# Kernel optimization log

Hardware: AMD Instinct MI355X
Metric: run time of the kernel (lower is better)

Reference implementation:

```python
import jax, jax.numpy as jnp
import numpy as np

N_HEAD = 8
LN_EPS = 1e-5


def _ln(z, g, b):
    m = jnp.mean(z, axis=-1, keepdims=True)
    v = jnp.var(z, axis=-1, keepdims=True)
    return (z - m) / jnp.sqrt(v + LN_EPS) * g + b


def setup_inputs() -> dict:
    key = jax.random.key(0)
    ks = jax.random.split(key, 20)
    B, N, H, F = 4, 256, 128, 512
    p = {}
    p["x"] = jax.random.normal(ks[0], (B, N, H), dtype=jnp.float32)
    p["e"] = jax.random.normal(ks[1], (B, N, N, H), dtype=jnp.float32)
    p["attention_mask"] = jnp.zeros((B, N_HEAD, N, N), dtype=jnp.float32)
    s = 0.02
    p["Wq"] = jax.random.normal(ks[2], (H, H)) * s; p["bq"] = jnp.zeros((H,))
    p["Wk"] = jax.random.normal(ks[3], (H, H)) * s; p["bk"] = jnp.zeros((H,))
    p["Wv"] = jax.random.normal(ks[4], (H, H)) * s; p["bv"] = jnp.zeros((H,))
    p["We"] = jax.random.normal(ks[5], (H, H)) * s; p["be"] = jnp.zeros((H,))
    p["Woh"] = jax.random.normal(ks[6], (H, H)) * s; p["boh"] = jnp.zeros((H,))
    p["Woe"] = jax.random.normal(ks[7], (H, H)) * s; p["boe"] = jnp.zeros((H,))
    p["Wf1x"] = jax.random.normal(ks[8], (H, F)) * s; p["bf1x"] = jnp.zeros((F,))
    p["Wf2x"] = jax.random.normal(ks[9], (F, H)) * s; p["bf2x"] = jnp.zeros((H,))
    p["Wf1e"] = jax.random.normal(ks[10], (H, F)) * s; p["bf1e"] = jnp.zeros((F,))
    p["Wf2e"] = jax.random.normal(ks[11], (F, H)) * s; p["bf2e"] = jnp.zeros((H,))
    p["g1x"] = jnp.ones((H,)); p["b1x"] = jnp.zeros((H,))
    p["g1e"] = jnp.ones((H,)); p["b1e"] = jnp.zeros((H,))
    return p


def reference(x, e, attention_mask, Wq, bq, Wk, bk, Wv, bv, We, be,
              Woh, boh, Woe, boe, Wf1x, bf1x, Wf2x, bf2x,
              Wf1e, bf1e, Wf2e, bf2e, g1x, b1x, g1e, b1e):
    B, N, H = x.shape
    h = N_HEAD
    d = H // h
    # projections; NOTE: V uses the K projection (faithful to original bug)
    Qx = (x @ Wq + bq).reshape(B, N, h, d).transpose(0, 2, 1, 3)   # (B,h,N,d)
    Kx = (x @ Wk + bk).reshape(B, N, h, d).transpose(0, 2, 1, 3)
    Vx = (x @ Wk + bk).reshape(B, N, h, d).transpose(0, 2, 1, 3)
    Ee = (e @ We + be).reshape(B, N, N, h, d).transpose(0, 3, 1, 2, 4)  # (B,h,N,N,d)
    scale = 1.0 / np.sqrt(d).astype(np.float32)
    inter = Qx[:, :, :, None, :] * Kx[:, :, None, :, :] * Ee * scale   # (B,h,N,N,d)
    scores = jax.nn.softmax(attention_mask + inter.sum(-1), axis=-1)   # (B,h,N,N)
    e_attn = inter.transpose(0, 2, 3, 1, 4).reshape(B, N, N, H) @ Woe + boe
    att = jnp.einsum('bhij,bhjd->bhid', scores, Vx)
    x_attn = att.transpose(0, 2, 1, 3).reshape(B, N, H) @ Woh + boh
    # residual + layernorm (original 'layer' path reuses normalization1_* twice)
    x1 = _ln(x_attn + x, g1x, b1x)
    e1 = _ln(e_attn + e, g1e, b1e)
    x_ff = jax.nn.relu(x1 @ Wf1x + bf1x) @ Wf2x + bf2x
    e_ff = jax.nn.relu(e1 @ Wf1e + bf1e) @ Wf2e + bf2e
    x2 = _ln(x_ff + x1, g1x, b1x)
    e2 = _ln(e_ff + e1, g1e, b1e)
    return x2, e2
```

## Files before the change

### kernel.cpp

```cpp
#include <hip/hip_runtime.h>
#include <math.h>

#define NSEQ 256
#define HD 128
#define FD 512
#define NHD 8
#define LNEPS 1e-5f

typedef __attribute__((ext_vector_type(8))) short bf16x8;
typedef __attribute__((ext_vector_type(4))) float f32x4;

__device__ __forceinline__ unsigned short f2bf(float x) {
  union { float f; unsigned int u; } v; v.f = x;
  unsigned int r = v.u + 0x7fffu + ((v.u >> 16) & 1u);
  return (unsigned short)(r >> 16);
}

__device__ __forceinline__ float bf2f(unsigned short u) {
  union { float f; unsigned int v; } cv; cv.v = ((unsigned int)u) << 16;
  return cv.f;
}

__global__ void prep_weights(const float* __restrict__ W1f, const float* __restrict__ W2f,
                             unsigned short* __restrict__ W1T, unsigned short* __restrict__ W2T) {
  int t = blockIdx.x * 256 + threadIdx.x;
  int tot = gridDim.x * 256;
  for (int idx = t; idx < FD * HD; idx += tot) {
    int n = idx >> 7, k = idx & (HD - 1);
    W1T[idx] = f2bf(W1f[k * FD + n]);
  }
  for (int idx = t; idx < HD * FD; idx += tot) {
    int n = idx >> 9, k = idx & (FD - 1);
    W2T[idx] = f2bf(W2f[k * HD + n]);
  }
}

__global__ __launch_bounds__(128) void qk_proj(const float* __restrict__ x,
    const float* __restrict__ Wq, const float* __restrict__ bq,
    const float* __restrict__ Wk, const float* __restrict__ bk,
    float* __restrict__ Qs, float* __restrict__ Kp) {
  int row = blockIdx.x;
  int c = threadIdx.x;
  __shared__ float xl[HD];
  xl[c] = x[row * HD + c];
  __syncthreads();
  float aq = bq[c], ak = bk[c];
  #pragma unroll 8
  for (int k = 0; k < HD; ++k) {
    float xv = xl[k];
    aq = fmaf(xv, Wq[k * HD + c], aq);
    ak = fmaf(xv, Wk[k * HD + c], ak);
  }
  Qs[row * HD + c] = aq * 0.25f;
  Kp[row * HD + c] = ak;
}

__global__ __launch_bounds__(256) void edge_attn(
    const float* __restrict__ e,
    const float* __restrict__ We, const float* __restrict__ be,
    const float* __restrict__ Woe, const float* __restrict__ boe,
    const float* __restrict__ Qs, const float* __restrict__ Kp,
    const float* __restrict__ g1e, const float* __restrict__ b1e,
    float* __restrict__ Sout, float* __restrict__ e1out) {
  const int gid = blockIdx.x;
  const int jt = gid & 3, i = (gid >> 2) & (NSEQ - 1), b = gid >> 10;
  const int j0 = jt * 64;
  const int t = threadIdx.x;
  const int w = t >> 6, l = t & 63;
  const int wr = w >> 1, wc = w & 1;
  const int l15 = l & 15, lg = l >> 4;

  __shared__ unsigned short eL[64 * 128];
  __shared__ unsigned short kL[64 * 136];
  __shared__ float qL[HD], beL[HD], boeL[HD], gL[HD], bbL[HD];
  __shared__ float redS[64][2], redQ[64][2];

  if (t < HD) {
    qL[t]   = Qs[(b * NSEQ + i) * HD + t];
    beL[t]  = be[t];
    boeL[t] = boe[t];
    gL[t]   = g1e[t];
    bbL[t]  = b1e[t];
  }
  const int ebase = ((b * NSEQ + i) * NSEQ + j0) * HD;
  for (int v = t; v < 64 * 16; v += 256) {
    int r = v >> 4, c8 = (v & 15) << 3;
    const float* se = &e[ebase + r * HD + c8];
    float4 e0 = *(const float4*)se;
    float4 e1v = *(const float4*)(se + 4);
    union { bf16x8 v8; unsigned short u[8]; } pk;
    pk.u[0] = f2bf(e0.x); pk.u[1] = f2bf(e0.y); pk.u[2] = f2bf(e0.z); pk.u[3] = f2bf(e0.w);
    pk.u[4] = f2bf(e1v.x); pk.u[5] = f2bf(e1v.y); pk.u[6] = f2bf(e1v.z); pk.u[7] = f2bf(e1v.w);
    *(bf16x8*)&eL[r * HD + (c8 ^ ((r & 7) << 3))] = pk.v8;
    const float* sk = &Kp[(b * NSEQ + j0 + r) * HD + c8];
    float4 k0 = *(const float4*)sk;
    float4 k1 = *(const float4*)(sk + 4);
    pk.u[0] = f2bf(k0.x); pk.u[1] = f2bf(k0.y); pk.u[2] = f2bf(k0.z); pk.u[3] = f2bf(k0.w);
    pk.u[4] = f2bf(k1.x); pk.u[5] = f2bf(k1.y); pk.u[6] = f2bf(k1.z); pk.u[7] = f2bf(k1.w);
    *(bf16x8*)&kL[r * 136 + c8] = pk.v8;
  }
  __syncthreads();

  f32x4 acc1[2][4];
  #pragma unroll
  for (int tm = 0; tm < 2; ++tm)
    #pragma unroll
    for (int tn = 0; tn < 4; ++tn) {
      float bv = beL[wc * 64 + tn * 16 + l15];
      acc1[tm][tn] = (f32x4){bv, bv, bv, bv};
    }
  #pragma unroll
  for (int ks = 0; ks < 4; ++ks) {
    bf16x8 af[2], bfr[4];
    #pragma unroll
    for (int tm = 0; tm < 2; ++tm) {
      int mrow = wr * 32 + tm * 16 + l15;
      af[tm] = *(const bf16x8*)&eL[mrow * HD + ((ks * 32 + lg * 8) ^ ((mrow & 7) << 3))];
    }
    #pragma unroll
    for (int tn = 0; tn < 4; ++tn) {
      int n = wc * 64 + tn * 16 + l15;
      const float* wp = &We[(ks * 32 + lg * 8) * HD + n];
      union { bf16x8 v8; unsigned short u[8]; } pk;
      #pragma unroll
      for (int ii = 0; ii < 8; ++ii) pk.u[ii] = f2bf(wp[ii * HD]);
      bfr[tn] = pk.v8;
    }
    #pragma unroll
    for (int tm = 0; tm < 2; ++tm)
      #pragma unroll
      for (int tn = 0; tn < 4; ++tn)
        acc1[tm][tn] = __builtin_amdgcn_mfma_f32_16x16x32_bf16(af[tm], bfr[tn], acc1[tm][tn], 0, 0, 0);
  }

  #pragma unroll
  for (int tm = 0; tm < 2; ++tm)
    #pragma unroll
    for (int tn = 0; tn < 4; ++tn) {
      int c = wc * 64 + tn * 16 + l15;
      float qv = qL[c];
      f32x4 p;
      #pragma unroll
      for (int ii = 0; ii < 4; ++ii) {
        int r = wr * 32 + tm * 16 + lg * 4 + ii;
        p[ii] = acc1[tm][tn][ii] * qv * bf2f(kL[r * 136 + c]);
      }
      acc1[tm][tn] = p;
      float h0 = p[0], h1 = p[1], h2 = p[2], h3 = p[3];
      #pragma unroll
      for (int off = 1; off < 16; off <<= 1) {
        h0 += __shfl_xor(h0, off); h1 += __shfl_xor(h1, off);
        h2 += __shfl_xor(h2, off); h3 += __shfl_xor(h3, off);
      }
      if (l15 < 4) {
        float val = l15 == 0 ? h0 : l15 == 1 ? h1 : l15 == 2 ? h2 : h3;
        int r = wr * 32 + tm * 16 + lg * 4 + l15;
        Sout[((b * NHD + (wc * 4 + tn)) * NSEQ + i) * NSEQ + j0 + r] = val;
      }
    }
  __syncthreads();

  #pragma unroll
  for (int tm = 0; tm < 2; ++tm)
    #pragma unroll
    for (int tn = 0; tn < 4; ++tn) {
      int c = wc * 64 + tn * 16 + l15;
      #pragma unroll
      for (int ii = 0; ii < 4; ++ii) {
        int r = wr * 32 + tm * 16 + lg * 4 + ii;
        eL[r * HD + (c ^ ((r & 7) << 3))] = f2bf(acc1[tm][tn][ii]);
      }
    }
  __syncthreads();

  f32x4 acc2[2][4];
  #pragma unroll
  for (int tm = 0; tm < 2; ++tm)
    #pragma unroll
    for (int tn = 0; tn < 4; ++tn) {
      float bv = boeL[wc * 64 + tn * 16 + l15];
      acc2[tm][tn] = (f32x4){bv, bv, bv, bv};
    }
  #pragma unroll
  for (int ks = 0; ks < 4; ++ks) {
    bf16x8 af[2], bfr[4];
    #pragma unroll
    for (int tm = 0; tm < 2; ++tm) {
      int mrow = wr * 32 + tm * 16 + l15;
      af[tm] = *(const bf16x8*)&eL[mrow * HD + ((ks * 32 + lg * 8) ^ ((mrow & 7) << 3))];
    }
    #pragma unroll
    for (int tn = 0; tn < 4; ++tn) {
      int n = wc * 64 + tn * 16 + l15;
      const float* wp = &Woe[(ks * 32 + lg * 8) * HD + n];
      union { bf16x8 v8; unsigned short u[8]; } pk;
      #pragma unroll
      for (int ii = 0; ii < 8; ++ii) pk.u[ii] = f2bf(wp[ii * HD]);
      bfr[tn] = pk.v8;
    }
    #pragma unroll
    for (int tm = 0; tm < 2; ++tm)
      #pragma unroll
      for (int tn = 0; tn < 4; ++tn)
        acc2[tm][tn] = __builtin_amdgcn_mfma_f32_16x16x32_bf16(af[tm], bfr[tn], acc2[tm][tn], 0, 0, 0);
  }

  #pragma unroll
  for (int tm = 0; tm < 2; ++tm) {
    #pragma unroll
    for (int tn = 0; tn < 4; ++tn) {
      int c = wc * 64 + tn * 16 + l15;
      #pragma unroll
      for (int ii = 0; ii < 4; ++ii) {
        int r = wr * 32 + tm * 16 + lg * 4 + ii;
        acc2[tm][tn][ii] += e[ebase + r * HD + c];
      }
    }
    #pragma unroll
    for (int ii = 0; ii < 4; ++ii) {
      float s  = acc2[tm][0][ii] + acc2[tm][1][ii] + acc2[tm][2][ii] + acc2[tm][3][ii];
      float sq = acc2[tm][0][ii] * acc2[tm][0][ii] + acc2[tm][1][ii] * acc2[tm][1][ii]
               + acc2[tm][2][ii] * acc2[tm][2][ii] + acc2[tm][3][ii] * acc2[tm][3][ii];
      #pragma unroll
      for (int off = 1; off < 16; off <<= 1) {
        s += __shfl_xor(s, off); sq += __shfl_xor(sq, off);
      }
      if (l15 == 0) {
        int r = wr * 32 + tm * 16 + lg * 4 + ii;
        redS[r][wc] = s; redQ[r][wc] = sq;
      }
    }
  }
  __syncthreads();

  #pragma unroll
  for (int tm = 0; tm < 2; ++tm) {
    float mrow[4], rsrow[4];
    #pragma unroll
    for (int ii = 0; ii < 4; ++ii) {
      int r = wr * 32 + tm * 16 + lg * 4 + ii;
      float s = redS[r][0] + redS[r][1];
      float sq = redQ[r][0] + redQ[r][1];
      float m = s * (1.f / HD);
      float var = sq * (1.f / HD) - m * m;
      mrow[ii] = m; rsrow[ii] = rsqrtf(var + LNEPS);
    }
    #pragma unroll
    for (int tn = 0; tn < 4; ++tn) {
      int c = wc * 64 + tn * 16 + l15;
      float gv = gL[c], bv = bbL[c];
      #pragma unroll
      for (int ii = 0; ii < 4; ++ii) {
        int r = wr * 32 + tm * 16 + lg * 4 + ii;
        e1out[ebase + r * HD + c] = (acc2[tm][tn][ii] - mrow[ii]) * rsrow[ii] * gv + bv;
      }
    }
  }
}

__global__ __launch_bounds__(256) void softmax_k(float* __restrict__ S,
    const float* __restrict__ mask) {
  int row = blockIdx.x;
  int t = threadIdx.x;
  int idx = row * NSEQ + t;
  float v = S[idx] + mask[idx];
  float m = v;
  #pragma unroll
  for (int off = 1; off < 64; off <<= 1) m = fmaxf(m, __shfl_xor(m, off));
  __shared__ float wbuf[8];
  if ((t & 63) == 0) wbuf[t >> 6] = m;
  __syncthreads();
  m = fmaxf(fmaxf(wbuf[0], wbuf[1]), fmaxf(wbuf[2], wbuf[3]));
  float ex = __expf(v - m);
  float s = ex;
  #pragma unroll
  for (int off = 1; off < 64; off <<= 1) s += __shfl_xor(s, off);
  __syncthreads();
  if ((t & 63) == 0) wbuf[4 + (t >> 6)] = s;
  __syncthreads();
  s = wbuf[4] + wbuf[5] + wbuf[6] + wbuf[7];
  S[idx] = ex / s;
}

__global__ __launch_bounds__(128) void x_attn_ln(
    const float* __restrict__ x, const float* __restrict__ scores,
    const float* __restrict__ Kp,
    const float* __restrict__ Woh, const float* __restrict__ boh,
    const float* __restrict__ g1x, const float* __restrict__ b1x,
    float* __restrict__ x1out) {
  int bi = blockIdx.x; int b = bi >> 8; int i = bi & 255;
  int c = threadIdx.x;
  __shared__ float sL[NHD * NSEQ];
  __shared__ float attL[HD];
  __shared__ float rbuf[4];

  for (int v = c; v < NHD * NSEQ; v += 128) {
    int h = v >> 8, j = v & 255;
    sL[v] = scores[((b * NHD + h) * NSEQ + i) * NSEQ + j];
  }
  __syncthreads();
  int h = c >> 4;
  float att = 0.f;
  for (int j = 0; j < NSEQ; ++j)
    att = fmaf(sL[h * NSEQ + j], Kp[(b * NSEQ + j) * HD + c], att);
  attL[c] = att;
  __syncthreads();
  float o = boh[c];
  for (int k = 0; k < HD; ++k) o = fmaf(attL[k], Woh[k * HD + c], o);
  o += x[bi * HD + c];
  float s = o, s2 = o * o;
  #pragma unroll
  for (int off = 1; off < 64; off <<= 1) { s += __shfl_xor(s, off); s2 += __shfl_xor(s2, off); }
  if ((c & 63) == 0) { rbuf[(c >> 6) * 2] = s; rbuf[(c >> 6) * 2 + 1] = s2; }
  __syncthreads();
  s = rbuf[0] + rbuf[2]; s2 = rbuf[1] + rbuf[3];
  float m = s * (1.f / HD);
  float var = s2 * (1.f / HD) - m * m;
  x1out[bi * HD + c] = (o - m) * rsqrtf(var + LNEPS) * g1x[c] + b1x[c];
}

__global__ __launch_bounds__(256) void ffn_mfma(
    const float* in1,
    const unsigned short* __restrict__ W1T, const float* __restrict__ b1,
    const unsigned short* __restrict__ W2T, const float* __restrict__ b2,
    const float* __restrict__ g, const float* __restrict__ bb,
    float* out2) {
  const int row0 = blockIdx.x * 64;
  const int t = threadIdx.x;
  const int w = t >> 6, l = t & 63;
  const int wr = w >> 1, wc = w & 1;
  const int l15 = l & 15, lg = l >> 4;

  __shared__ __align__(16) char smem[34816];
  unsigned short* aL = (unsigned short*)smem;
  unsigned short* hL = (unsigned short*)(smem + 16384);
  float* b1L = (float*)(smem + 32768);
  float* epi = (float*)smem;

  for (int v = t; v < 64 * 16; v += 256) {
    int r = v >> 4, c8 = (v & 15) << 3;
    const float* src = &in1[(row0 + r) * HD + c8];
    float4 f0 = *(const float4*)src;
    float4 f1 = *(const float4*)(src + 4);
    union { bf16x8 v8; unsigned short u[8]; } pk;
    pk.u[0] = f2bf(f0.x); pk.u[1] = f2bf(f0.y); pk.u[2] = f2bf(f0.z); pk.u[3] = f2bf(f0.w);
    pk.u[4] = f2bf(f1.x); pk.u[5] = f2bf(f1.y); pk.u[6] = f2bf(f1.z); pk.u[7] = f2bf(f1.w);
    *(bf16x8*)&aL[r * HD + (c8 ^ ((r & 7) << 3))] = pk.v8;
  }
  for (int v = t; v < FD; v += 256) b1L[v] = b1[v];
  __syncthreads();

  f32x4 acc2[2][4];
  #pragma unroll
  for (int tm = 0; tm < 2; ++tm)
    #pragma unroll
    for (int tn = 0; tn < 4; ++tn) acc2[tm][tn] = (f32x4){0.f, 0.f, 0.f, 0.f};

  for (int fc = 0; fc < 4; ++fc) {
    f32x4 acc1[2][4];
    #pragma unroll
    for (int tm = 0; tm < 2; ++tm)
      #pragma unroll
      for (int tn = 0; tn < 4; ++tn) acc1[tm][tn] = (f32x4){0.f, 0.f, 0.f, 0.f};
    #pragma unroll
    for (int ks = 0; ks < 4; ++ks) {
      bf16x8 af[2], bfr[4];
      #pragma unroll
      for (int tm = 0; tm < 2; ++tm) {
        int mrow = wr * 32 + tm * 16 + l15;
        af[tm] = *(const bf16x8*)&aL[mrow * HD + ((ks * 32 + lg * 8) ^ ((mrow & 7) << 3))];
      }
      #pragma unroll
      for (int tn = 0; tn < 4; ++tn) {
        int n = fc * 128 + wc * 64 + tn * 16 + l15;
        bfr[tn] = *(const bf16x8*)&W1T[n * HD + ks * 32 + lg * 8];
      }
      #pragma unroll
      for (int tm = 0; tm < 2; ++tm)
        #pragma unroll
        for (int tn = 0; tn < 4; ++tn)
          acc1[tm][tn] = __builtin_amdgcn_mfma_f32_16x16x32_bf16(af[tm], bfr[tn], acc1[tm][tn], 0, 0, 0);
    }
    __syncthreads();
    #pragma unroll
    for (int tm = 0; tm < 2; ++tm)
      #pragma unroll
      for (int tn = 0; tn < 4; ++tn) {
        int col = wc * 64 + tn * 16 + l15;
        float bias = b1L[fc * 128 + col];
        #pragma unroll
        for (int ii = 0; ii < 4; ++ii) {
          int r = wr * 32 + tm * 16 + lg * 4 + ii;
          float hv = fmaxf(acc1[tm][tn][ii] + bias, 0.f);
          hL[r * HD + (col ^ ((r & 7) << 3))] = f2bf(hv);
        }
      }
    __syncthreads();
    #pragma unroll
    for (int ks = 0; ks < 4; ++ks) {
      bf16x8 af[2], bfr[4];
      #pragma unroll
      for (int tm = 0; tm < 2; ++tm) {
        int mrow = wr * 32 + tm * 16 + l15;
        af[tm] = *(const bf16x8*)&hL[mrow * HD + ((ks * 32 + lg * 8) ^ ((mrow & 7) << 3))];
      }
      #pragma unroll
      for (int tn = 0; tn < 4; ++tn) {
        int n = wc * 64 + tn * 16 + l15;
        bfr[tn] = *(const bf16x8*)&W2T[n * FD + fc * 128 + ks * 32 + lg * 8];
      }
      #pragma unroll
      for (int tm = 0; tm < 2; ++tm)
        #pragma unroll
        for (int tn = 0; tn < 4; ++tn)
          acc2[tm][tn] = __builtin_amdgcn_mfma_f32_16x16x32_bf16(af[tm], bfr[tn], acc2[tm][tn], 0, 0, 0);
    }
  }

  float res[2][4][4];
  #pragma unroll
  for (int tm = 0; tm < 2; ++tm)
    #pragma unroll
    for (int tn = 0; tn < 4; ++tn) {
      int col = wc * 64 + tn * 16 + l15;
      #pragma unroll
      for (int ii = 0; ii < 4; ++ii) {
        int r = wr * 32 + tm * 16 + lg * 4 + ii;
        res[tm][tn][ii] = bf2f(aL[r * HD + (col ^ ((r & 7) << 3))]);
      }
    }
  __syncthreads();

  #pragma unroll
  for (int tm = 0; tm < 2; ++tm)
    #pragma unroll
    for (int tn = 0; tn < 4; ++tn) {
      int col = wc * 64 + tn * 16 + l15;
      float bias = b2[col];
      #pragma unroll
      for (int ii = 0; ii < 4; ++ii) {
        int r = wr * 32 + tm * 16 + lg * 4 + ii;
        epi[r * 132 + col] = acc2[tm][tn][ii] + bias + res[tm][tn][ii];
      }
    }
  __syncthreads();
  {
    int r = t >> 2, sgi = t & 3;
    const float* rowp = &epi[r * 132 + sgi * 32];
    float sum = 0.f, sq = 0.f;
    #pragma unroll
    for (int u = 0; u < 32; u += 4) {
      float4 v4 = *(const float4*)&rowp[u];
      sum += v4.x + v4.y + v4.z + v4.w;
      sq  += v4.x * v4.x + v4.y * v4.y + v4.z * v4.z + v4.w * v4.w;
    }
    sum += __shfl_xor(sum, 1); sq += __shfl_xor(sq, 1);
    sum += __shfl_xor(sum, 2); sq += __shfl_xor(sq, 2);
    float m = sum * (1.f / HD);
    float var = sq * (1.f / HD) - m * m;
    float rs = rsqrtf(var + LNEPS);
    #pragma unroll
    for (int u = 0; u < 32; u += 4) {
      float4 v4 = *(const float4*)&rowp[u];
      int cb = sgi * 32 + u;
      float4 o;
      o.x = (v4.x - m) * rs * g[cb + 0] + bb[cb + 0];
      o.y = (v4.y - m) * rs * g[cb + 1] + bb[cb + 1];
      o.z = (v4.z - m) * rs * g[cb + 2] + bb[cb + 2];
      o.w = (v4.w - m) * rs * g[cb + 3] + bb[cb + 3];
      *(float4*)&out2[(row0 + r) * HD + cb] = o;
    }
  }
}

__global__ __launch_bounds__(256) void ffn_mfma_e(
    const float* in1,
    const float* __restrict__ W1, const float* __restrict__ b1,
    const float* __restrict__ W2, const float* __restrict__ b2,
    const float* __restrict__ g, const float* __restrict__ bb,
    float* out2) {
  const int t = threadIdx.x;
  const int w = t >> 6, l = t & 63;
  const int wr = w >> 1, wc = w & 1;
  const int l15 = l & 15, lg = l >> 4;
  const int rowbase = blockIdx.x * 512;

  __shared__ __align__(16) char smem[69632];
  unsigned short* aL = (unsigned short*)smem;
  unsigned short* hL = (unsigned short*)(smem + 16384);
  float* b1L = (float*)(smem + 32768);
  float* epi = (float*)(smem + 34816);

  for (int v = t; v < FD; v += 256) b1L[v] = b1[v];

  for (int ch = 0; ch < 8; ++ch) {
    const int row0 = rowbase + ch * 64;
    __syncthreads();

    for (int v = t; v < 64 * 16; v += 256) {
      int r = v >> 4, c8 = (v & 15) << 3;
      const float* src = &in1[(row0 + r) * HD + c8];
      float4 f0 = *(const float4*)src;
      float4 f1 = *(const float4*)(src + 4);
      union { bf16x8 v8; unsigned short u[8]; } pk;
      pk.u[0] = f2bf(f0.x); pk.u[1] = f2bf(f0.y); pk.u[2] = f2bf(f0.z); pk.u[3] = f2bf(f0.w);
      pk.u[4] = f2bf(f1.x); pk.u[5] = f2bf(f1.y); pk.u[6] = f2bf(f1.z); pk.u[7] = f2bf(f1.w);
      *(bf16x8*)&aL[r * HD + (c8 ^ ((r & 7) << 3))] = pk.v8;
    }
    __syncthreads();

    f32x4 acc2[2][4];
    #pragma unroll
    for (int tm = 0; tm < 2; ++tm)
      #pragma unroll
      for (int tn = 0; tn < 4; ++tn) acc2[tm][tn] = (f32x4){0.f, 0.f, 0.f, 0.f};

    for (int fc = 0; fc < 4; ++fc) {
      f32x4 acc1[2][4];
      #pragma unroll
      for (int tm = 0; tm < 2; ++tm)
        #pragma unroll
        for (int tn = 0; tn < 4; ++tn) acc1[tm][tn] = (f32x4){0.f, 0.f, 0.f, 0.f};
      #pragma unroll
      for (int ks = 0; ks < 4; ++ks) {
        bf16x8 af[2], bfr[4];
        #pragma unroll
        for (int tm = 0; tm < 2; ++tm) {
          int mrow = wr * 32 + tm * 16 + l15;
          af[tm] = *(const bf16x8*)&aL[mrow * HD + ((ks * 32 + lg * 8) ^ ((mrow & 7) << 3))];
        }
        #pragma unroll
        for (int tn = 0; tn < 4; ++tn) {
          int n = fc * 128 + wc * 64 + tn * 16 + l15;
          const float* wp = &W1[(ks * 32 + lg * 8) * FD + n];
          union { bf16x8 v8; unsigned short u[8]; } pk;
          #pragma unroll
          for (int i = 0; i < 8; ++i) pk.u[i] = f2bf(wp[i * FD]);
          bfr[tn] = pk.v8;
        }
        #pragma unroll
        for (int tm = 0; tm < 2; ++tm)
          #pragma unroll
          for (int tn = 0; tn < 4; ++tn)
            acc1[tm][tn] = __builtin_amdgcn_mfma_f32_16x16x32_bf16(af[tm], bfr[tn], acc1[tm][tn], 0, 0, 0);
      }
      __syncthreads();
      #pragma unroll
      for (int tm = 0; tm < 2; ++tm)
        #pragma unroll
        for (int tn = 0; tn < 4; ++tn) {
          int col = wc * 64 + tn * 16 + l15;
          float bias = b1L[fc * 128 + col];
          #pragma unroll
          for (int ii = 0; ii < 4; ++ii) {
            int r = wr * 32 + tm * 16 + lg * 4 + ii;
            float hv = fmaxf(acc1[tm][tn][ii] + bias, 0.f);
            hL[r * HD + (col ^ ((r & 7) << 3))] = f2bf(hv);
          }
        }
      __syncthreads();
      #pragma unroll
      for (int ks = 0; ks < 4; ++ks) {
        bf16x8 af[2], bfr[4];
        #pragma unroll
        for (int tm = 0; tm < 2; ++tm) {
          int mrow = wr * 32 + tm * 16 + l15;
          af[tm] = *(const bf16x8*)&hL[mrow * HD + ((ks * 32 + lg * 8) ^ ((mrow & 7) << 3))];
        }
        #pragma unroll
        for (int tn = 0; tn < 4; ++tn) {
          int n = wc * 64 + tn * 16 + l15;
          const float* wp = &W2[(fc * 128 + ks * 32 + lg * 8) * HD + n];
          union { bf16x8 v8; unsigned short u[8]; } pk;
          #pragma unroll
          for (int i = 0; i < 8; ++i) pk.u[i] = f2bf(wp[i * HD]);
          bfr[tn] = pk.v8;
        }
        #pragma unroll
        for (int tm = 0; tm < 2; ++tm)
          #pragma unroll
          for (int tn = 0; tn < 4; ++tn)
            acc2[tm][tn] = __builtin_amdgcn_mfma_f32_16x16x32_bf16(af[tm], bfr[tn], acc2[tm][tn], 0, 0, 0);
      }
    }

    #pragma unroll
    for (int tm = 0; tm < 2; ++tm)
      #pragma unroll
      for (int tn = 0; tn < 4; ++tn) {
        int col = wc * 64 + tn * 16 + l15;
        float bias = b2[col];
        #pragma unroll
        for (int ii = 0; ii < 4; ++ii) {
          int r = wr * 32 + tm * 16 + lg * 4 + ii;
          float rv = bf2f(aL[r * HD + (col ^ ((r & 7) << 3))]);
          epi[r * 132 + col] = acc2[tm][tn][ii] + bias + rv;
        }
      }
    __syncthreads();
    {
      int r = t >> 2, sgi = t & 3;
      const float* rowp = &epi[r * 132 + sgi * 32];
      float sum = 0.f, sq = 0.f;
      #pragma unroll
      for (int u = 0; u < 32; u += 4) {
        float4 v4 = *(const float4*)&rowp[u];
        sum += v4.x + v4.y + v4.z + v4.w;
        sq  += v4.x * v4.x + v4.y * v4.y + v4.z * v4.z + v4.w * v4.w;
      }
      sum += __shfl_xor(sum, 1); sq += __shfl_xor(sq, 1);
      sum += __shfl_xor(sum, 2); sq += __shfl_xor(sq, 2);
      float m = sum * (1.f / HD);
      float var = sq * (1.f / HD) - m * m;
      float rs = rsqrtf(var + LNEPS);
      #pragma unroll
      for (int u = 0; u < 32; u += 4) {
        float4 v4 = *(const float4*)&rowp[u];
        int cb = sgi * 32 + u;
        float4 o;
        o.x = (v4.x - m) * rs * g[cb + 0] + bb[cb + 0];
        o.y = (v4.y - m) * rs * g[cb + 1] + bb[cb + 1];
        o.z = (v4.z - m) * rs * g[cb + 2] + bb[cb + 2];
        o.w = (v4.w - m) * rs * g[cb + 3] + bb[cb + 3];
        *(float4*)&out2[(row0 + r) * HD + cb] = o;
      }
    }
  }
}

extern "C" void kernel_launch(void* const* d_in, const int* in_sizes, int n_in,
                              void* d_out, int out_size, void* d_ws, size_t ws_size,
                              hipStream_t stream) {
  const float* x    = (const float*)d_in[0];
  const float* e    = (const float*)d_in[1];
  const float* mask = (const float*)d_in[2];
  const float* Wq   = (const float*)d_in[3];
  const float* bq   = (const float*)d_in[4];
  const float* Wk   = (const float*)d_in[5];
  const float* bk   = (const float*)d_in[6];
  const float* We   = (const float*)d_in[9];
  const float* be   = (const float*)d_in[10];
  const float* Woh  = (const float*)d_in[11];
  const float* boh  = (const float*)d_in[12];
  const float* Woe  = (const float*)d_in[13];
  const float* boe  = (const float*)d_in[14];
  const float* Wf1x = (const float*)d_in[15];
  const float* bf1x = (const float*)d_in[16];
  const float* Wf2x = (const float*)d_in[17];
  const float* bf2x = (const float*)d_in[18];
  const float* Wf1e = (const float*)d_in[19];
  const float* bf1e = (const float*)d_in[20];
  const float* Wf2e = (const float*)d_in[21];
  const float* bf2e = (const float*)d_in[22];
  const float* g1x  = (const float*)d_in[23];
  const float* b1x  = (const float*)d_in[24];
  const float* g1e  = (const float*)d_in[25];
  const float* b1e  = (const float*)d_in[26];

  float* xout = (float*)d_out;
  float* eout = (float*)d_out + 131072;

  char* ws = (char*)d_ws;
  unsigned short* W1Tx = (unsigned short*)(ws);
  unsigned short* W2Tx = (unsigned short*)(ws + 131072);
  float* Qs  = (float*)(ws + 262144);
  float* Kp  = (float*)(ws + 786432);
  float* x1b = (float*)(ws + 1310720);
  float* S   = (float*)(ws + 1835008);

  prep_weights<<<64, 256, 0, stream>>>(Wf1x, Wf2x, W1Tx, W2Tx);
  qk_proj<<<1024, 128, 0, stream>>>(x, Wq, bq, Wk, bk, Qs, Kp);
  edge_attn<<<4096, 256, 0, stream>>>(e, We, be, Woe, boe, Qs, Kp, g1e, b1e, S, eout);
  softmax_k<<<8192, 256, 0, stream>>>(S, mask);
  x_attn_ln<<<1024, 128, 0, stream>>>(x, S, Kp, Woh, boh, g1x, b1x, x1b);
  ffn_mfma<<<16, 256, 0, stream>>>(x1b, W1Tx, bf1x, W2Tx, bf2x, g1x, b1x, xout);
  ffn_mfma_e<<<512, 256, 0, stream>>>(eout, Wf1e, bf1e, Wf2e, bf2e, g1e, b1e, eout);
}
```

Before: 433.9 us.

## Double FFN edge row tile to 128 and do LayerNorm in registers

The edge FFN kernel now processes 128 rows per chunk instead of 64, so each wave computes a 64x64 tile. Every W1/W2 fragment it loads from global memory and converts to bf16 is reused across twice as many rows. The residual LayerNorm now reduces row statistics with shuffles and a small shared buffer instead of staging the whole output tile in shared memory. A cheaper round-to-nearest bf16 conversion without tie-to-even replaces the old one. In exchange, register pressure doubles for the accumulators, the output stores become less coalesced scalar writes, and rounding changes slightly.

After: 467.8 us. 7.8% more time.

```diff
diff --git a/kernel.cpp b/kernel.cpp
--- a/kernel.cpp
+++ b/kernel.cpp
@@ -14,6 +14,11 @@
   union { float f; unsigned int u; } v; v.f = x;
   unsigned int r = v.u + 0x7fffu + ((v.u >> 16) & 1u);
   return (unsigned short)(r >> 16);
+}
+
+__device__ __forceinline__ unsigned short f2bf_c(float x) {
+  union { float f; unsigned int u; } v; v.f = x;
+  return (unsigned short)((v.u + 0x8000u) >> 16);
 }
 
 __device__ __forceinline__ float bf2f(unsigned short u) {
@@ -487,46 +492,47 @@
 
   __shared__ __align__(16) char smem[69632];
   unsigned short* aL = (unsigned short*)smem;
-  unsigned short* hL = (unsigned short*)(smem + 16384);
-  float* b1L = (float*)(smem + 32768);
-  float* epi = (float*)(smem + 34816);
+  unsigned short* hL = (unsigned short*)(smem + 32768);
+  float* b1L  = (float*)(smem + 65536);
+  float* redS = (float*)(smem + 67584);
+  float* redQ = (float*)(smem + 68608);
 
   for (int v = t; v < FD; v += 256) b1L[v] = b1[v];
 
-  for (int ch = 0; ch < 8; ++ch) {
-    const int row0 = rowbase + ch * 64;
+  for (int ch = 0; ch < 4; ++ch) {
+    const int row0 = rowbase + ch * 128;
     __syncthreads();
 
-    for (int v = t; v < 64 * 16; v += 256) {
+    for (int v = t; v < 128 * 16; v += 256) {
       int r = v >> 4, c8 = (v & 15) << 3;
       const float* src = &in1[(row0 + r) * HD + c8];
       float4 f0 = *(const float4*)src;
       float4 f1 = *(const float4*)(src + 4);
       union { bf16x8 v8; unsigned short u[8]; } pk;
-      pk.u[0] = f2bf(f0.x); pk.u[1] = f2bf(f0.y); pk.u[2] = f2bf(f0.z); pk.u[3] = f2bf(f0.w);
-      pk.u[4] = f2bf(f1.x); pk.u[5] = f2bf(f1.y); pk.u[6] = f2bf(f1.z); pk.u[7] = f2bf(f1.w);
+      pk.u[0] = f2bf_c(f0.x); pk.u[1] = f2bf_c(f0.y); pk.u[2] = f2bf_c(f0.z); pk.u[3] = f2bf_c(f0.w);
+      pk.u[4] = f2bf_c(f1.x); pk.u[5] = f2bf_c(f1.y); pk.u[6] = f2bf_c(f1.z); pk.u[7] = f2bf_c(f1.w);
       *(bf16x8*)&aL[r * HD + (c8 ^ ((r & 7) << 3))] = pk.v8;
     }
     __syncthreads();
 
-    f32x4 acc2[2][4];
-    #pragma unroll
-    for (int tm = 0; tm < 2; ++tm)
+    f32x4 acc2[4][4];
+    #pragma unroll
+    for (int tm = 0; tm < 4; ++tm)
       #pragma unroll
       for (int tn = 0; tn < 4; ++tn) acc2[tm][tn] = (f32x4){0.f, 0.f, 0.f, 0.f};
 
     for (int fc = 0; fc < 4; ++fc) {
-      f32x4 acc1[2][4];
-      #pragma unroll
-      for (int tm = 0; tm < 2; ++tm)
+      f32x4 acc1[4][4];
+      #pragma unroll
+      for (int tm = 0; tm < 4; ++tm)
         #pragma unroll
         for (int tn = 0; tn < 4; ++tn) acc1[tm][tn] = (f32x4){0.f, 0.f, 0.f, 0.f};
       #pragma unroll
       for (int ks = 0; ks < 4; ++ks) {
-        bf16x8 af[2], bfr[4];
-        #pragma unroll
-        for (int tm = 0; tm < 2; ++tm) {
-          int mrow = wr * 32 + tm * 16 + l15;
+        bf16x8 af[4], bfr[4];
+        #pragma unroll
+        for (int tm = 0; tm < 4; ++tm) {
+          int mrow = wr * 64 + tm * 16 + l15;
           af[tm] = *(const bf16x8*)&aL[mrow * HD + ((ks * 32 + lg * 8) ^ ((mrow & 7) << 3))];
         }
         #pragma unroll
@@ -535,36 +541,36 @@
           const float* wp = &W1[(ks * 32 + lg * 8) * FD + n];
           union { bf16x8 v8; unsigned short u[8]; } pk;
           #pragma unroll
-          for (int i = 0; i < 8; ++i) pk.u[i] = f2bf(wp[i * FD]);
+          for (int i = 0; i < 8; ++i) pk.u[i] = f2bf_c(wp[i * FD]);
           bfr[tn] = pk.v8;
         }
         #pragma unroll
-        for (int tm = 0; tm < 2; ++tm)
+        for (int tm = 0; tm < 4; ++tm)
           #pragma unroll
           for (int tn = 0; tn < 4; ++tn)
             acc1[tm][tn] = __builtin_amdgcn_mfma_f32_16x16x32_bf16(af[tm], bfr[tn], acc1[tm][tn], 0, 0, 0);
       }
       __syncthreads();
       #pragma unroll
-      for (int tm = 0; tm < 2; ++tm)
+      for (int tm = 0; tm < 4; ++tm)
         #pragma unroll
         for (int tn = 0; tn < 4; ++tn) {
           int col = wc * 64 + tn * 16 + l15;
           float bias = b1L[fc * 128 + col];
           #pragma unroll
           for (int ii = 0; ii < 4; ++ii) {
-            int r = wr * 32 + tm * 16 + lg * 4 + ii;
+            int r = wr * 64 + tm * 16 + lg * 4 + ii;
             float hv = fmaxf(acc1[tm][tn][ii] + bias, 0.f);
-            hL[r * HD + (col ^ ((r & 7) << 3))] = f2bf(hv);
+            hL[r * HD + (col ^ ((r & 7) << 3))] = f2bf_c(hv);
           }
         }
       __syncthreads();
       #pragma unroll
       for (int ks = 0; ks < 4; ++ks) {
-        bf16x8 af[2], bfr[4];
-        #pragma unroll
-        for (int tm = 0; tm < 2; ++tm) {
-          int mrow = wr * 32 + tm * 16 + l15;
+        bf16x8 af[4], bfr[4];
+        #pragma unroll
+        for (int tm = 0; tm < 4; ++tm) {
+          int mrow = wr * 64 + tm * 16 + l15;
           af[tm] = *(const bf16x8*)&hL[mrow * HD + ((ks * 32 + lg * 8) ^ ((mrow & 7) << 3))];
         }
         #pragma unroll
@@ -573,11 +579,11 @@
           const float* wp = &W2[(fc * 128 + ks * 32 + lg * 8) * HD + n];
           union { bf16x8 v8; unsigned short u[8]; } pk;
           #pragma unroll
-          for (int i = 0; i < 8; ++i) pk.u[i] = f2bf(wp[i * HD]);
+          for (int i = 0; i < 8; ++i) pk.u[i] = f2bf_c(wp[i * HD]);
           bfr[tn] = pk.v8;
         }
         #pragma unroll
-        for (int tm = 0; tm < 2; ++tm)
+        for (int tm = 0; tm < 4; ++tm)
           #pragma unroll
           for (int tn = 0; tn < 4; ++tn)
             acc2[tm][tn] = __builtin_amdgcn_mfma_f32_16x16x32_bf16(af[tm], bfr[tn], acc2[tm][tn], 0, 0, 0);
@@ -585,44 +591,55 @@
     }
 
     #pragma unroll
-    for (int tm = 0; tm < 2; ++tm)
+    for (int tm = 0; tm < 4; ++tm) {
       #pragma unroll
       for (int tn = 0; tn < 4; ++tn) {
         int col = wc * 64 + tn * 16 + l15;
         float bias = b2[col];
         #pragma unroll
         for (int ii = 0; ii < 4; ++ii) {
-          int r = wr * 32 + tm * 16 + lg * 4 + ii;
-          float rv = bf2f(aL[r * HD + (col ^ ((r & 7) << 3))]);
-          epi[r * 132 + col] = acc2[tm][tn][ii] + bias + rv;
-        }
-      }
+          int r = wr * 64 + tm * 16 + lg * 4 + ii;
+          acc2[tm][tn][ii] += bias + bf2f(aL[r * HD + (col ^ ((r & 7) << 3))]);
+        }
+      }
+      #pragma unroll
+      for (int ii = 0; ii < 4; ++ii) {
+        float s  = acc2[tm][0][ii] + acc2[tm][1][ii] + acc2[tm][2][ii] + acc2[tm][3][ii];
+        float sq = acc2[tm][0][ii] * acc2[tm][0][ii] + acc2[tm][1][ii] * acc2[tm][1][ii]
+                 + acc2[tm][2][ii] * acc2[tm][2][ii] + acc2[tm][3][ii] * acc2[tm][3][ii];
+        #pragma unroll
+        for (int off = 1; off < 16; off <<= 1) {
+          s += __shfl_xor(s, off); sq += __shfl_xor(sq, off);
+        }
+        if (l15 == 0) {
+          int r = wr * 64 + tm * 16 + lg * 4 + ii;
+          redS[r * 2 + wc] = s; redQ[r * 2 + wc] = sq;
+        }
+      }
+    }
     __syncthreads();
-    {
-      int r = t >> 2, sgi = t & 3;
-      const float* rowp = &epi[r * 132 + sgi * 32];
-      float sum = 0.f, sq = 0.f;
-      #pragma unroll
-      for (int u = 0; u < 32; u += 4) {
-        float4 v4 = *(const float4*)&rowp[u];
-        sum += v4.x + v4.y + v4.z + v4.w;
-        sq  += v4.x * v4.x + v4.y * v4.y + v4.z * v4.z + v4.w * v4.w;
-      }
-      sum += __shfl_xor(sum, 1); sq += __shfl_xor(sq, 1);
-      sum += __shfl_xor(sum, 2); sq += __shfl_xor(sq, 2);
-      float m = sum * (1.f / HD);
-      float var = sq * (1.f / HD) - m * m;
-      float rs = rsqrtf(var + LNEPS);
-      #pragma unroll
-      for (int u = 0; u < 32; u += 4) {
-        float4 v4 = *(const float4*)&rowp[u];
-        int cb = sgi * 32 + u;
-        float4 o;
-        o.x = (v4.x - m) * rs * g[cb + 0] + bb[cb + 0];
-        o.y = (v4.y - m) * rs * g[cb + 1] + bb[cb + 1];
-        o.z = (v4.z - m) * rs * g[cb + 2] + bb[cb + 2];
-        o.w = (v4.w - m) * rs * g[cb + 3] + bb[cb + 3];
-        *(float4*)&out2[(row0 + r) * HD + cb] = o;
+
+    #pragma unroll
+    for (int tm = 0; tm < 4; ++tm) {
+      float mrow[4], rsrow[4];
+      #pragma unroll
+      for (int ii = 0; ii < 4; ++ii) {
+        int r = wr * 64 + tm * 16 + lg * 4 + ii;
+        float s = redS[r * 2] + redS[r * 2 + 1];
+        float sq = redQ[r * 2] + redQ[r * 2 + 1];
+        float m = s * (1.f / HD);
+        float var = sq * (1.f / HD) - m * m;
+        mrow[ii] = m; rsrow[ii] = rsqrtf(var + LNEPS);
+      }
+      #pragma unroll
+      for (int tn = 0; tn < 4; ++tn) {
+        int col = wc * 64 + tn * 16 + l15;
+        float gv = g[col], bv = bb[col];
+        #pragma unroll
+        for (int ii = 0; ii < 4; ++ii) {
+          int r = wr * 64 + tm * 16 + lg * 4 + ii;
+          out2[(row0 + r) * HD + col] = (acc2[tm][tn][ii] - mrow[ii]) * rsrow[ii] * gv + bv;
+        }
       }
     }
   }
```
